# Optimization experiments

Measured on AMD Instinct MI355X. Metric: run time of the kernel, lower is better.

The kernel has to match this reference:

```python
import jax, jax.numpy as jnp
import numpy as np

B, HW, C, H = 4, 2048, 768, 8
HD = C // H  # 96


def _rotate_half_interleaved(t):
    # t: [..., HD]; pairs (t1, t2) at even/odd positions -> (-t2, t1) interleaved
    t1 = t[..., ::2]
    t2 = t[..., 1::2]
    return jnp.stack([-t2, t1], axis=-1).reshape(t.shape)


def setup_inputs() -> dict:
    key = jax.random.key(0)
    kx, kq, kp, kb = jax.random.split(key, 4)
    x = jax.random.normal(kx, (B, HW, C), dtype=jnp.float32)
    # standard interleaved RoPE tables: freq repeated pairwise along head_dim
    inv_freq = 1.0 / (10000.0 ** (np.arange(0, HD, 2, dtype=np.float32) / HD))  # [HD/2]
    angles = np.arange(HW, dtype=np.float32)[:, None] * inv_freq[None, :]        # [HW, HD/2]
    angles = np.repeat(angles, 2, axis=-1)                                        # [HW, HD]
    cos = jnp.asarray(np.cos(angles), dtype=jnp.float32)
    sin = jnp.asarray(np.sin(angles), dtype=jnp.float32)
    Wqkv = jax.random.normal(kq, (3 * C, C), dtype=jnp.float32) * (C ** -0.5)
    Wproj = jax.random.normal(kp, (C, C), dtype=jnp.float32) * (C ** -0.5)
    bproj = jnp.zeros((C,), dtype=jnp.float32)
    return {"x": x, "cos": cos, "sin": sin, "Wqkv": Wqkv, "Wproj": Wproj, "bproj": bproj}


def reference(x, cos, sin, Wqkv, Wproj, bproj):
    Bv, hw, Cv = x.shape
    scale = HD ** -0.5
    qkv = x @ Wqkv.T                                  # [B, hw, 3C]
    qkv = qkv.reshape(Bv, hw, 3, H, HD).transpose(2, 0, 3, 1, 4)  # [3, B, H, hw, HD]
    q, k, v = qkv[0], qkv[1], qkv[2]
    # RoPE: broadcast cos/sin [hw, HD] over [B, H, hw, HD]
    cosb = cos[None, None, :, :]
    sinb = sin[None, None, :, :]
    q = q * cosb + _rotate_half_interleaved(q) * sinb
    k = k * cosb + _rotate_half_interleaved(k) * sinb
    attn = jnp.einsum('bhqd,bhkd->bhqk', q, k) * scale
    attn = jax.nn.softmax(attn, axis=-1)
    out = jnp.einsum('bhqk,bhkd->bhqd', attn, v)      # [B, H, hw, HD]
    out = out.transpose(0, 2, 1, 3).reshape(Bv, hw, Cv)
    return out @ Wproj.T + bproj
```

## Files before the change

kernel.cpp:

```cpp
#include <hip/hip_runtime.h>
#include <hip/hip_bf16.h>
#include <math.h>

#define Bc  4
#define HWc 2048
#define Cc  768
#define Hc  8
#define HDc 96

typedef short bf16x8 __attribute__((ext_vector_type(8)));
typedef float f32x4  __attribute__((ext_vector_type(4)));

static __device__ __forceinline__ unsigned short f2bf(float x) {
    __hip_bfloat16 h = __float2bfloat16(x);
    return *reinterpret_cast<unsigned short*>(&h);
}

#define GLOBAL_AS(p) ((const __attribute__((address_space(1))) void*)(p))
#define LDS_AS(p)    ((__attribute__((address_space(3))) void*)(p))

__global__ __launch_bounds__(256) void cast_all(
    const float* __restrict__ x, const float* __restrict__ Wq,
    const float* __restrict__ Wp, unsigned short* __restrict__ xb,
    unsigned short* __restrict__ Wqb, unsigned short* __restrict__ Wpb,
    int nx4, int nwq4, int nwp4)
{
    int i = blockIdx.x * 256 + threadIdx.x;
    const float* src; unsigned short* dst; int j = i;
    if (i < nx4) { src = x; dst = xb; }
    else if ((j = i - nx4) < nwq4) { src = Wq; dst = Wqb; }
    else if ((j = i - nx4 - nwq4) < nwp4) { src = Wp; dst = Wpb; }
    else return;
    float4 v = ((const float4*)src)[j];
    ushort4 p;
    p.x = f2bf(v.x); p.y = f2bf(v.y); p.z = f2bf(v.z); p.w = f2bf(v.w);
    ((ushort4*)dst)[j] = p;
}

__global__ __launch_bounds__(256) void qkv_mfma_T(
    const unsigned short* __restrict__ Wb, const unsigned short* __restrict__ xb,
    const float* __restrict__ cs, const float* __restrict__ sn,
    unsigned short* __restrict__ qo, unsigned short* __restrict__ ko,
    unsigned short* __restrict__ vt)
{
    __shared__ unsigned short Al[128 * 32];
    __shared__ unsigned short Bl[128 * 32];
    __shared__ unsigned short Tt[64][132];
    const int tid  = threadIdx.x;
    const int lane = tid & 63;
    const int w    = tid >> 6;
    const int c    = lane & 15, qd = lane >> 4;
    const int wm   = w & 1, wn = w >> 1;
    const int m0   = blockIdx.y << 7;
    const int n0   = blockIdx.x << 7;

    const int srow = (w << 5) + (lane >> 2);
    const int sseg = (lane & 3) << 3;
    const unsigned short* Ag = Wb + (size_t)(m0 + srow) * Cc + sseg;
    const unsigned short* Bg = xb + (size_t)(n0 + srow) * Cc + sseg;
    unsigned short* Adst = &Al[(w << 5) * 32];
    unsigned short* Bdst = &Bl[(w << 5) * 32];

    f32x4 acc[4][4];
    #pragma unroll
    for (int i = 0; i < 4; i++)
        #pragma unroll
        for (int j = 0; j < 4; j++) acc[i][j] = (f32x4)0.f;

    for (int k0 = 0; k0 < Cc; k0 += 32) {
        __syncthreads();
        __builtin_amdgcn_global_load_lds(GLOBAL_AS(Ag + k0),            LDS_AS(Adst),            16, 0, 0);
        __builtin_amdgcn_global_load_lds(GLOBAL_AS(Ag + 16 * Cc + k0),  LDS_AS(Adst + 16 * 32),  16, 0, 0);
        __builtin_amdgcn_global_load_lds(GLOBAL_AS(Bg + k0),            LDS_AS(Bdst),            16, 0, 0);
        __builtin_amdgcn_global_load_lds(GLOBAL_AS(Bg + 16 * Cc + k0),  LDS_AS(Bdst + 16 * 32),  16, 0, 0);
        __syncthreads();

        bf16x8 af[4], bfr[4];
        #pragma unroll
        for (int mt = 0; mt < 4; mt++)
            af[mt] = *(const bf16x8*)&Al[((wm << 6) + mt * 16 + c) * 32 + qd * 8];
        #pragma unroll
        for (int nt = 0; nt < 4; nt++)
            bfr[nt] = *(const bf16x8*)&Bl[((wn << 6) + nt * 16 + c) * 32 + qd * 8];
        #pragma unroll
        for (int mt = 0; mt < 4; mt++)
            #pragma unroll
            for (int nt = 0; nt < 4; nt++)
                acc[mt][nt] = __builtin_amdgcn_mfma_f32_16x16x32_bf16(
                    af[mt], bfr[nt], acc[mt][nt], 0, 0, 0);
    }

    const int which = m0 / Cc;
    const int m0l = m0 - which * Cc;
    const float qs = 0.10206207261596577f;

    if (which == 2) {
        #pragma unroll
        for (int mt = 0; mt < 4; mt++) {
            const int c0 = m0l + (wm << 6) + mt * 16 + (qd << 2);
            const int h = c0 / HDc, d = c0 % HDc;
            #pragma unroll
            for (int nt = 0; nt < 4; nt++) {
                const int t = n0 + (wn << 6) + nt * 16 + c;
                const int b = t >> 11, tt = t & (HWc - 1);
                const size_t base = ((size_t)((b * Hc + h) * HDc + d)) * HWc + tt;
                #pragma unroll
                for (int r = 0; r < 4; r++)
                    vt[base + (size_t)r * HWc] = f2bf(acc[mt][nt][r]);
            }
        }
    } else {
        unsigned short* dst = which ? ko : qo;
        const float sc = which ? 1.0f : qs;
        for (int tk = 0; tk < 2; tk++) {
            __syncthreads();
            if (wn == tk) {
                #pragma unroll
                for (int mt = 0; mt < 4; mt++) {
                    const int c0 = m0l + (wm << 6) + mt * 16 + (qd << 2);
                    const int d = c0 % HDc;
                    #pragma unroll
                    for (int nt = 0; nt < 4; nt++) {
                        const int t = n0 + (wn << 6) + nt * 16 + c;
                        const int tt = t & (HWc - 1);
                        const float4 c4 = *(const float4*)&cs[tt * HDc + d];
                        const float4 s4 = *(const float4*)&sn[tt * HDc + d];
                        float o0 = (acc[mt][nt][0] * c4.x - acc[mt][nt][1] * s4.x) * sc;
                        float o1 = (acc[mt][nt][1] * c4.y + acc[mt][nt][0] * s4.y) * sc;
                        float o2 = (acc[mt][nt][2] * c4.z - acc[mt][nt][3] * s4.z) * sc;
                        float o3 = (acc[mt][nt][3] * c4.w + acc[mt][nt][2] * s4.w) * sc;
                        ushort4 pk;
                        pk.x = f2bf(o0); pk.y = f2bf(o1);
                        pk.z = f2bf(o2); pk.w = f2bf(o3);
                        *(ushort4*)&Tt[nt * 16 + c][(wm << 6) + mt * 16 + (qd << 2)] = pk;
                    }
                }
            }
            __syncthreads();
            #pragma unroll
            for (int it = 0; it < 8; it++) {
                int s = tid + (it << 8);
                int row = s >> 5, fseg = (s & 31) << 2;
                int fg = m0l + fseg;
                int h = fg / HDc, d = fg % HDc;
                int token = n0 + tk * 64 + row;
                int b = token >> 11, tt = token & (HWc - 1);
                *(ushort4*)&dst[((size_t)(b * Hc + h) * HWc + tt) * HDc + d] =
                    *(ushort4*)&Tt[row][fseg];
            }
        }
    }
}

__global__ __launch_bounds__(256, 4) void attn_flash(
    const unsigned short* __restrict__ qg, const unsigned short* __restrict__ kg,
    const unsigned short* __restrict__ vtg, unsigned short* __restrict__ ob)
{
    __shared__ unsigned short Ks[64][96];
    __shared__ unsigned short Vt[96][64];
    __shared__ unsigned short Pt[4][16][72];

    const int tid  = threadIdx.x;
    const int lane = tid & 63;
    const int w    = tid >> 6;
    const int c    = lane & 15;
    const int qd   = lane >> 4;
    const int bh   = blockIdx.x;
    const int b    = bh >> 3, h = bh & 7;
    const int q0   = blockIdx.y << 6;

    const unsigned short* kb  = kg  + (size_t)bh * HWc * HDc;
    const unsigned short* vtb = vtg + (size_t)bh * HDc * HWc;

    bf16x8 qt[3];
    {
        const unsigned short* qr = qg + ((size_t)bh * HWc + q0 + w * 16 + c) * HDc + qd * 8;
        #pragma unroll
        for (int ks = 0; ks < 3; ks++)
            qt[ks] = *(const bf16x8*)(qr + ks * 32);
    }

    unsigned short* Kbase = &Ks[0][0];
    unsigned short* Vbase = &Vt[0][0];
    const int vrow_l = lane >> 3;
    const int vseg_l = ((lane & 7) ^ vrow_l) << 3;

    f32x4 oacc[6];
    #pragma unroll
    for (int mt = 0; mt < 6; mt++) oacc[mt] = (f32x4)0.f;
    float lsum = 0.f;

    {
        const unsigned short* kc = kb;
        #pragma unroll
        for (int it = 0; it < 3; it++) {
            const int chunk = w * 3 + it;
            __builtin_amdgcn_global_load_lds(
                GLOBAL_AS(kc + chunk * 512 + lane * 8),
                LDS_AS(Kbase + chunk * 512), 16, 0, 0);
        }
    }

    for (int ck = 0; ck < 32; ck++) {
        __syncthreads();
        {
            const unsigned short* vc = vtb + (ck << 6);
            #pragma unroll
            for (int it = 0; it < 3; it++) {
                const int chunk = w * 3 + it;
                __builtin_amdgcn_global_load_lds(
                    GLOBAL_AS(vc + (size_t)(chunk * 8 + vrow_l) * HWc + vseg_l),
                    LDS_AS(Vbase + chunk * 512), 16, 0, 0);
            }
        }

        f32x4 sacc[4];
        #pragma unroll
        for (int mt = 0; mt < 4; mt++) sacc[mt] = (f32x4)0.f;
        __builtin_amdgcn_s_setprio(1);
        #pragma unroll
        for (int mt = 0; mt < 4; mt++)
            #pragma unroll
            for (int ks = 0; ks < 3; ks++) {
                bf16x8 af = *(const bf16x8*)&Ks[mt * 16 + c][ks * 32 + qd * 8];
                sacc[mt] = __builtin_amdgcn_mfma_f32_16x16x32_bf16(
                    af, qt[ks], sacc[mt], 0, 0, 0);
            }
        __builtin_amdgcn_s_setprio(0);

        __syncthreads();
        if (ck < 31) {
            const unsigned short* kc = kb + (size_t)((ck + 1) << 6) * HDc;
            #pragma unroll
            for (int it = 0; it < 3; it++) {
                const int chunk = w * 3 + it;
                __builtin_amdgcn_global_load_lds(
                    GLOBAL_AS(kc + chunk * 512 + lane * 8),
                    LDS_AS(Kbase + chunk * 512), 16, 0, 0);
            }
        }

        float rs = 0.f;
        #pragma unroll
        for (int mt = 0; mt < 4; mt++)
            #pragma unroll
            for (int r = 0; r < 4; r++) {
                float p = __expf(sacc[mt][r]);
                sacc[mt][r] = p;
                rs += p;
            }
        rs += __shfl_xor(rs, 16);
        rs += __shfl_xor(rs, 32);
        lsum += rs;

        #pragma unroll
        for (int mt = 0; mt < 4; mt++) {
            __hip_bfloat162 p01 = __float22bfloat162_rn(float2{sacc[mt][0], sacc[mt][1]});
            __hip_bfloat162 p23 = __float22bfloat162_rn(float2{sacc[mt][2], sacc[mt][3]});
            uint2 pk;
            pk.x = *reinterpret_cast<unsigned int*>(&p01);
            pk.y = *reinterpret_cast<unsigned int*>(&p23);
            *(uint2*)&Pt[w][c][mt * 16 + qd * 4] = pk;
        }
        bf16x8 pf[2];
        #pragma unroll
        for (int ks = 0; ks < 2; ks++)
            pf[ks] = *(const bf16x8*)&Pt[w][c][ks * 32 + qd * 8];

        __builtin_amdgcn_s_setprio(1);
        #pragma unroll
        for (int mt = 0; mt < 6; mt++)
            #pragma unroll
            for (int ks = 0; ks < 2; ks++) {
                const int row = mt * 16 + c;
                bf16x8 vf = *(const bf16x8*)&Vt[row][(((ks << 2) + qd) ^ (c & 7)) << 3];
                oacc[mt] = __builtin_amdgcn_mfma_f32_16x16x32_bf16(
                    vf, pf[ks], oacc[mt], 0, 0, 0);
            }
        __builtin_amdgcn_s_setprio(0);
    }

    const float linv = 1.0f / lsum;
    unsigned short* orow = ob + ((size_t)(b * HWc + q0 + w * 16 + c)) * Cc + h * HDc;
    #pragma unroll
    for (int mt = 0; mt < 6; mt++) {
        f32x4 val = oacc[mt] * linv;
        ushort4 pk;
        pk.x = f2bf(val[0]); pk.y = f2bf(val[1]);
        pk.z = f2bf(val[2]); pk.w = f2bf(val[3]);
        *(ushort4*)&orow[mt * 16 + qd * 4] = pk;
    }
}

__global__ __launch_bounds__(256) void proj_mfma_T64(
    const unsigned short* __restrict__ Wb, const unsigned short* __restrict__ Ab,
    const float* __restrict__ bias, float* __restrict__ out)
{
    __shared__ unsigned short Al[128 * 32];
    __shared__ unsigned short Bl[64 * 32];
    const int tid  = threadIdx.x;
    const int lane = tid & 63;
    const int w    = tid >> 6;
    const int c    = lane & 15, qd = lane >> 4;
    const int wm   = w & 1, wn = w >> 1;
    const int m0   = blockIdx.y << 7;
    const int n0   = blockIdx.x << 6;

    const int srow = (w << 5) + (lane >> 2);
    const int sseg = (lane & 3) << 3;
    const unsigned short* Ag = Wb + (size_t)(m0 + srow) * Cc + sseg;
    unsigned short* Adst = &Al[(w << 5) * 32];
    const int brow = (w << 4) + (lane >> 2);
    const unsigned short* Bg = Ab + (size_t)(n0 + brow) * Cc + sseg;
    unsigned short* Bdst = &Bl[(w << 4) * 32];

    f32x4 acc[4][2];
    #pragma unroll
    for (int i = 0; i < 4; i++)
        #pragma unroll
        for (int j = 0; j < 2; j++) acc[i][j] = (f32x4)0.f;

    for (int k0 = 0; k0 < Cc; k0 += 32) {
        __syncthreads();
        __builtin_amdgcn_global_load_lds(GLOBAL_AS(Ag + k0),           LDS_AS(Adst),           16, 0, 0);
        __builtin_amdgcn_global_load_lds(GLOBAL_AS(Ag + 16 * Cc + k0), LDS_AS(Adst + 16 * 32), 16, 0, 0);
        __builtin_amdgcn_global_load_lds(GLOBAL_AS(Bg + k0),           LDS_AS(Bdst),           16, 0, 0);
        __syncthreads();

        bf16x8 af[4], bfr[2];
        #pragma unroll
        for (int mt = 0; mt < 4; mt++)
            af[mt] = *(const bf16x8*)&Al[((wm << 6) + mt * 16 + c) * 32 + qd * 8];
        #pragma unroll
        for (int nt = 0; nt < 2; nt++)
            bfr[nt] = *(const bf16x8*)&Bl[((wn << 5) + nt * 16 + c) * 32 + qd * 8];
        #pragma unroll
        for (int mt = 0; mt < 4; mt++)
            #pragma unroll
            for (int nt = 0; nt < 2; nt++)
                acc[mt][nt] = __builtin_amdgcn_mfma_f32_16x16x32_bf16(
                    af[mt], bfr[nt], acc[mt][nt], 0, 0, 0);
    }

    #pragma unroll
    for (int mt = 0; mt < 4; mt++) {
        const int f = m0 + (wm << 6) + mt * 16 + (qd << 2);
        const float4 b4 = *(const float4*)&bias[f];
        #pragma unroll
        for (int nt = 0; nt < 2; nt++) {
            const int t = n0 + (wn << 5) + nt * 16 + c;
            float4 val;
            val.x = acc[mt][nt][0] + b4.x;
            val.y = acc[mt][nt][1] + b4.y;
            val.z = acc[mt][nt][2] + b4.z;
            val.w = acc[mt][nt][3] + b4.w;
            *(float4*)&out[(size_t)t * Cc + f] = val;
        }
    }
}

extern "C" void kernel_launch(void* const* d_in, const int* in_sizes, int n_in,
                              void* d_out, int out_size, void* d_ws, size_t ws_size,
                              hipStream_t stream) {
    const float* x     = (const float*)d_in[0];
    const float* cs    = (const float*)d_in[1];
    const float* sn    = (const float*)d_in[2];
    const float* Wqkv  = (const float*)d_in[3];
    const float* Wproj = (const float*)d_in[4];
    const float* bproj = (const float*)d_in[5];
    float* out = (float*)d_out;

    const size_t per = (size_t)Bc * Hc * HWc * HDc;
    const size_t nx  = per;
    const size_t nwq = (size_t)3 * Cc * Cc;
    const size_t nwp = (size_t)Cc * Cc;

    unsigned short* xb  = (unsigned short*)d_ws;
    unsigned short* Wqb = xb + nx;
    unsigned short* Wpb = Wqb + nwq;
    unsigned short* q   = Wpb + nwp;
    unsigned short* k   = q + per;
    unsigned short* vt  = k + per;
    unsigned short* ob  = vt + per;

    const int nx4 = (int)(nx / 4), nwq4 = (int)(nwq / 4), nwp4 = (int)(nwp / 4);
    const int ntot = nx4 + nwq4 + nwp4;
    cast_all<<<dim3((ntot + 255) / 256), 256, 0, stream>>>(
        x, Wqkv, Wproj, xb, Wqb, Wpb, nx4, nwq4, nwp4);

    qkv_mfma_T<<<dim3(64, 18), 256, 0, stream>>>(Wqb, xb, cs, sn, q, k, vt);
    attn_flash<<<dim3(32, 32), 256, 0, stream>>>(q, k, vt, ob);
    proj_mfma_T64<<<dim3(128, 6), 256, 0, stream>>>(Wpb, ob, bproj, out);
}
```

Measured before the change: 269.1 us.

## Load GEMM fragments directly from global memory, dropping LDS staging and barriers

The QKV and projection GEMM kernels no longer stage A/B tiles into shared memory through global_load_lds with two barriers per k-step. Each wave now reads its MFMA fragments straight from global memory into registers, the k-loop is unrolled by two, and s_setprio is raised around the MFMA block. This removes barrier and LDS traffic, but each tile row is now fetched redundantly by several waves and the loads are strided, so the kernels lean on L1/L2 hits for reuse.

```diff
diff --git a/kernel.cpp b/kernel.cpp
--- a/kernel.cpp
+++ b/kernel.cpp
@@ -43,9 +43,8 @@
     unsigned short* __restrict__ qo, unsigned short* __restrict__ ko,
     unsigned short* __restrict__ vt)
 {
-    __shared__ unsigned short Al[128 * 32];
-    __shared__ unsigned short Bl[128 * 32];
     __shared__ unsigned short Tt[64][132];
+
     const int tid  = threadIdx.x;
     const int lane = tid & 63;
     const int w    = tid >> 6;
@@ -54,12 +53,8 @@
     const int m0   = blockIdx.y << 7;
     const int n0   = blockIdx.x << 7;
 
-    const int srow = (w << 5) + (lane >> 2);
-    const int sseg = (lane & 3) << 3;
-    const unsigned short* Ag = Wb + (size_t)(m0 + srow) * Cc + sseg;
-    const unsigned short* Bg = xb + (size_t)(n0 + srow) * Cc + sseg;
-    unsigned short* Adst = &Al[(w << 5) * 32];
-    unsigned short* Bdst = &Bl[(w << 5) * 32];
+    const unsigned short* Ap = Wb + (size_t)(m0 + (wm << 6) + c) * Cc + (qd << 3);
+    const unsigned short* Bp = xb + (size_t)(n0 + (wn << 6) + c) * Cc + (qd << 3);
 
     f32x4 acc[4][4];
     #pragma unroll
@@ -67,27 +62,23 @@
         #pragma unroll
         for (int j = 0; j < 4; j++) acc[i][j] = (f32x4)0.f;
 
+    #pragma unroll 2
     for (int k0 = 0; k0 < Cc; k0 += 32) {
-        __syncthreads();
-        __builtin_amdgcn_global_load_lds(GLOBAL_AS(Ag + k0),            LDS_AS(Adst),            16, 0, 0);
-        __builtin_amdgcn_global_load_lds(GLOBAL_AS(Ag + 16 * Cc + k0),  LDS_AS(Adst + 16 * 32),  16, 0, 0);
-        __builtin_amdgcn_global_load_lds(GLOBAL_AS(Bg + k0),            LDS_AS(Bdst),            16, 0, 0);
-        __builtin_amdgcn_global_load_lds(GLOBAL_AS(Bg + 16 * Cc + k0),  LDS_AS(Bdst + 16 * 32),  16, 0, 0);
-        __syncthreads();
-
         bf16x8 af[4], bfr[4];
         #pragma unroll
         for (int mt = 0; mt < 4; mt++)
-            af[mt] = *(const bf16x8*)&Al[((wm << 6) + mt * 16 + c) * 32 + qd * 8];
+            af[mt] = *(const bf16x8*)(Ap + (size_t)mt * 16 * Cc + k0);
         #pragma unroll
         for (int nt = 0; nt < 4; nt++)
-            bfr[nt] = *(const bf16x8*)&Bl[((wn << 6) + nt * 16 + c) * 32 + qd * 8];
+            bfr[nt] = *(const bf16x8*)(Bp + (size_t)nt * 16 * Cc + k0);
+        __builtin_amdgcn_s_setprio(1);
         #pragma unroll
         for (int mt = 0; mt < 4; mt++)
             #pragma unroll
             for (int nt = 0; nt < 4; nt++)
                 acc[mt][nt] = __builtin_amdgcn_mfma_f32_16x16x32_bf16(
                     af[mt], bfr[nt], acc[mt][nt], 0, 0, 0);
+        __builtin_amdgcn_s_setprio(0);
     }
 
     const int which = m0 / Cc;
@@ -296,8 +287,6 @@
     const unsigned short* __restrict__ Wb, const unsigned short* __restrict__ Ab,
     const float* __restrict__ bias, float* __restrict__ out)
 {
-    __shared__ unsigned short Al[128 * 32];
-    __shared__ unsigned short Bl[64 * 32];
     const int tid  = threadIdx.x;
     const int lane = tid & 63;
     const int w    = tid >> 6;
@@ -306,13 +295,8 @@
     const int m0   = blockIdx.y << 7;
     const int n0   = blockIdx.x << 6;
 
-    const int srow = (w << 5) + (lane >> 2);
-    const int sseg = (lane & 3) << 3;
-    const unsigned short* Ag = Wb + (size_t)(m0 + srow) * Cc + sseg;
-    unsigned short* Adst = &Al[(w << 5) * 32];
-    const int brow = (w << 4) + (lane >> 2);
-    const unsigned short* Bg = Ab + (size_t)(n0 + brow) * Cc + sseg;
-    unsigned short* Bdst = &Bl[(w << 4) * 32];
+    const unsigned short* Ap = Wb + (size_t)(m0 + (wm << 6) + c) * Cc + (qd << 3);
+    const unsigned short* Bp = Ab + (size_t)(n0 + (wn << 5) + c) * Cc + (qd << 3);
 
     f32x4 acc[4][2];
     #pragma unroll
@@ -320,26 +304,23 @@
         #pragma unroll
         for (int j = 0; j < 2; j++) acc[i][j] = (f32x4)0.f;
 
+    #pragma unroll 2
     for (int k0 = 0; k0 < Cc; k0 += 32) {
-        __syncthreads();
-        __builtin_amdgcn_global_load_lds(GLOBAL_AS(Ag + k0),           LDS_AS(Adst),           16, 0, 0);
-        __builtin_amdgcn_global_load_lds(GLOBAL_AS(Ag + 16 * Cc + k0), LDS_AS(Adst + 16 * 32), 16, 0, 0);
-        __builtin_amdgcn_global_load_lds(GLOBAL_AS(Bg + k0),           LDS_AS(Bdst),           16, 0, 0);
-        __syncthreads();
-
         bf16x8 af[4], bfr[2];
         #pragma unroll
         for (int mt = 0; mt < 4; mt++)
-            af[mt] = *(const bf16x8*)&Al[((wm << 6) + mt * 16 + c) * 32 + qd * 8];
+            af[mt] = *(const bf16x8*)(Ap + (size_t)mt * 16 * Cc + k0);
         #pragma unroll
         for (int nt = 0; nt < 2; nt++)
-            bfr[nt] = *(const bf16x8*)&Bl[((wn << 5) + nt * 16 + c) * 32 + qd * 8];
+            bfr[nt] = *(const bf16x8*)(Bp + (size_t)nt * 16 * Cc + k0);
+        __builtin_amdgcn_s_setprio(1);
         #pragma unroll
         for (int mt = 0; mt < 4; mt++)
             #pragma unroll
             for (int nt = 0; nt < 2; nt++)
                 acc[mt][nt] = __builtin_amdgcn_mfma_f32_16x16x32_bf16(
                     af[mt], bfr[nt], acc[mt][nt], 0, 0, 0);
+        __builtin_amdgcn_s_setprio(0);
     }
 
     #pragma unroll
```

New measurement: 336.3 us. +25.0%, slower.
